# Kernel tuning notes

Hardware: AMD Instinct MI355X
Metric: run time of the kernel (lower is better)

## Reference

```python
import jax, jax.numpy as jnp
import numpy as np

B, N, DIN, DOUT, EIN, EOUT = 8, 256, 64, 64, 64, 64


def setup_inputs() -> dict:
    key = jax.random.key(0)
    ks = jax.random.split(key, 9)
    A = jax.random.randint(ks[0], (B, N, N), 0, 2).astype(jnp.float32)  # {0,1} connectivity
    emb_node = jax.random.normal(ks[1], (B, N, DIN), dtype=jnp.float32)
    emb_edge = jax.random.normal(ks[2], (B, N, N, EIN), dtype=jnp.float32)
    s_n = 1.0 / np.sqrt(DIN)
    s_e = 1.0 / np.sqrt(EIN)
    Wn = jax.random.uniform(ks[3], (DIN, DOUT), minval=-s_n, maxval=s_n)
    bn = jax.random.uniform(ks[4], (DOUT,), minval=-s_n, maxval=s_n)
    Wsn = jax.random.uniform(ks[5], (DIN, DOUT), minval=-s_n, maxval=s_n)
    bsn = jax.random.uniform(ks[6], (DOUT,), minval=-s_n, maxval=s_n)
    We = jax.random.uniform(ks[7], (EIN, EOUT), minval=-s_e, maxval=s_e)
    be = jax.random.uniform(ks[8], (EOUT,), minval=-s_e, maxval=s_e)
    return {"A": A, "emb_node": emb_node, "emb_edge": emb_edge,
            "Wn": Wn, "bn": bn, "Wsn": Wsn, "bsn": bsn, "We": We, "be": be}


def reference(A, emb_node, emb_edge, Wn, bn, Wsn, bsn, We, be):
    # mode=1 (default) of ChannelIndependentConv
    node_x = emb_node @ Wn + bn          # [B,N,DOUT]
    node_sx = emb_node @ Wsn + bsn       # [B,N,DOUT]
    edge_x = emb_edge @ We + be          # [B,N,N,EOUT]
    # mask edges by connectivity, then channel-independent aggregation:
    # out[b,i,c] = sum_j A[b,i,j] * edge_x[b,i,j,c] * node_x[b,j,c]
    Ae = A[..., None] * edge_x           # [B,N,N,EOUT]
    agg = jnp.einsum('bijc,bjc->bic', Ae, node_x)  # [B,N,DOUT]
    node_out = jax.nn.relu(agg) + jax.nn.relu(node_sx)
    edge_out = jax.nn.relu(edge_x)
    return node_out, edge_out
```

## Files before the change

kernel.cpp:

```cpp
#include <hip/hip_runtime.h>
#include <hip/hip_bf16.h>

#define BN   2048
#define NN   256
#define CH   64
#define RPC  32
#define NCHK 8
#define LDST 88

typedef __attribute__((ext_vector_type(8))) short short8;
typedef __attribute__((ext_vector_type(4))) short short4v;
typedef __attribute__((ext_vector_type(4))) float fv4;

static __device__ inline short f2bf(float f) {
  unsigned u = __float_as_uint(f);
  u += 0x7FFF + ((u >> 16) & 1);
  return (short)(u >> 16);
}
static __device__ inline short4v cvt4(fv4 v) {
  short4v r;
  r[0] = f2bf(v[0]); r[1] = f2bf(v[1]); r[2] = f2bf(v[2]); r[3] = f2bf(v[3]);
  return r;
}

__global__ __launch_bounds__(256) void node_kernel(
    const float* __restrict__ emb_node, const float* __restrict__ Wn,
    const float* __restrict__ bn, const float* __restrict__ Wsn,
    const float* __restrict__ bsn, float* __restrict__ node_x,
    float* __restrict__ rsx) {
  __shared__ float s_emb[4][CH];
  __shared__ float s_Wn[CH * CH];
  __shared__ float s_Ws[CH * CH];
  const int tid = threadIdx.x;
  const int r = tid >> 6;
  const int c = tid & 63;
  const int row = blockIdx.x * 4 + r;
#pragma unroll
  for (int i = 0; i < 4; ++i) {
    *(fv4*)&s_Wn[(i * 256 + tid) * 4] = *(const fv4*)&Wn[(i * 256 + tid) * 4];
    *(fv4*)&s_Ws[(i * 256 + tid) * 4] = *(const fv4*)&Wsn[(i * 256 + tid) * 4];
  }
  s_emb[r][c] = emb_node[row * CH + c];
  __syncthreads();
  float a1 = bn[c], a2 = bsn[c];
#pragma unroll
  for (int k = 0; k < CH; ++k) {
    const float e = s_emb[r][k];
    a1 = fmaf(e, s_Wn[k * CH + c], a1);
    a2 = fmaf(e, s_Ws[k * CH + c], a2);
  }
  node_x[row * CH + c] = a1;
  rsx[row * CH + c] = fmaxf(a2, 0.0f);
}

__global__ __launch_bounds__(256) void edge_mfma_kernel(
    const float* __restrict__ A, const float* __restrict__ emb_edge,
    const float* __restrict__ We, const float* __restrict__ be,
    const float* __restrict__ node_x, const float* __restrict__ rsx,
    float* __restrict__ node_out, float* __restrict__ edge_out) {
  const int bi   = blockIdx.x;
  const int b    = bi >> 8;
  const int tid  = threadIdx.x;
  const int lane = tid & 63;
  const int wave = tid >> 6;
  const int l15  = lane & 15;
  const int quad = lane >> 4;
  const int c    = wave * 16 + l15;

  __shared__ __align__(16) short sbuf[2][RPC * LDST];
  __shared__ float s_A[NN];

  short8 bfrag[2];
#pragma unroll
  for (int h = 0; h < 2; ++h)
#pragma unroll
    for (int j = 0; j < 8; ++j)
      bfrag[h][j] = f2bf(We[(h * 32 + quad * 8 + j) * CH + c]);
  const float bias = be[c];

  const float* __restrict__ ee = emb_edge + (size_t)bi * NN * CH;
  float*       __restrict__ eo = edge_out + (size_t)bi * NN * CH;
  const float* __restrict__ nx = node_x + (size_t)b * NN * CH;

  s_A[tid] = A[(size_t)bi * NN + tid];

  const int srow = tid >> 4;
  const int kcol = (tid & 15) * 4;

  fv4 st0 = *(const fv4*)(ee + tid * 4);
  fv4 st1 = *(const fv4*)(ee + 1024 + tid * 4);
  *(short4v*)&sbuf[0][srow * LDST + kcol] = cvt4(st0);
  *(short4v*)&sbuf[0][(16 + srow) * LDST + kcol] = cvt4(st1);

  float agg = 0.0f;

#pragma unroll 2
  for (int ch = 0; ch < NCHK; ++ch) {
    const int pb = ch & 1;
    if (ch + 1 < NCHK) {
      const float* cb = ee + (ch + 1) * (RPC * CH);
      st0 = *(const fv4*)(cb + tid * 4);
      st1 = *(const fv4*)(cb + 1024 + tid * 4);
    }
    __syncthreads();

#pragma unroll
    for (int half = 0; half < 2; ++half) {
      const int j0l = half * 16;
      const int j0  = ch * RPC + j0l;
      const fv4 av = *(const fv4*)&s_A[j0 + quad * 4];
      float nxv[4];
#pragma unroll
      for (int r = 0; r < 4; ++r)
        nxv[r] = nx[(j0 + quad * 4 + r) * CH + c];
      const short8 af0 =
          *(const short8*)&sbuf[pb][(j0l + l15) * LDST + quad * 8];
      const short8 af1 =
          *(const short8*)&sbuf[pb][(j0l + l15) * LDST + 32 + quad * 8];
      fv4 acc = {0.0f, 0.0f, 0.0f, 0.0f};
      acc = __builtin_amdgcn_mfma_f32_16x16x32_bf16(af0, bfrag[0], acc, 0, 0, 0);
      acc = __builtin_amdgcn_mfma_f32_16x16x32_bf16(af1, bfrag[1], acc, 0, 0, 0);
#pragma unroll
      for (int r = 0; r < 4; ++r) {
        const int row = j0 + quad * 4 + r;
        const float ex = acc[r] + bias;
        eo[row * CH + c] = fmaxf(ex, 0.0f);
        agg = fmaf(av[r] * ex, nxv[r], agg);
      }
    }

    if (ch + 1 < NCHK) {
      *(short4v*)&sbuf[pb ^ 1][srow * LDST + kcol] = cvt4(st0);
      *(short4v*)&sbuf[pb ^ 1][(16 + srow) * LDST + kcol] = cvt4(st1);
    }
  }

  agg += __shfl_xor(agg, 16, 64);
  agg += __shfl_xor(agg, 32, 64);
  if (quad == 0) {
    node_out[(size_t)bi * CH + c] =
        fmaxf(agg, 0.0f) + rsx[(size_t)bi * CH + c];
  }
}

extern "C" void kernel_launch(void* const* d_in, const int* in_sizes, int n_in,
                              void* d_out, int out_size, void* d_ws, size_t ws_size,
                              hipStream_t stream) {
  const float* A        = (const float*)d_in[0];
  const float* emb_node = (const float*)d_in[1];
  const float* emb_edge = (const float*)d_in[2];
  const float* Wn       = (const float*)d_in[3];
  const float* bn       = (const float*)d_in[4];
  const float* Wsn      = (const float*)d_in[5];
  const float* bsn      = (const float*)d_in[6];
  const float* We       = (const float*)d_in[7];
  const float* be       = (const float*)d_in[8];

  float* node_out = (float*)d_out;
  float* edge_out = (float*)d_out + (size_t)BN * CH;

  float* node_x = (float*)d_ws;
  float* rsx    = (float*)d_ws + (size_t)BN * CH;

  hipLaunchKernelGGL(node_kernel, dim3(BN / 4), dim3(256), 0, stream,
                     emb_node, Wn, bn, Wsn, bsn, node_x, rsx);
  hipLaunchKernelGGL(edge_mfma_kernel, dim3(BN), dim3(256), 0, stream,
                     A, emb_edge, We, be, node_x, rsx, node_out, edge_out);
}
```

Before: 258.0 us.

## Split edge rows across waves, load A-fragments directly, drop LDS staging

Restructures the edge kernel so each wave owns 64 rows and computes all 64 output channels. The wave loads its emb_edge fragments straight from global memory into registers and converts them to bf16 there, which removes the LDS double buffer and the per-chunk barriers. The bias is folded into the accumulator init, edge_out uses nontemporal stores, and a small LDS reduction combines the per-wave aggregates at the end. The cost is more registers for four sets of We fragments and scattered 32-byte global loads in place of coalesced staging loads.

Result: slower. 273.6 us (+6.1%).

```diff
diff --git a/kernel.cpp b/kernel.cpp
--- a/kernel.cpp
+++ b/kernel.cpp
@@ -1,15 +1,10 @@
 #include <hip/hip_runtime.h>
-#include <hip/hip_bf16.h>
 
 #define BN   2048
 #define NN   256
 #define CH   64
-#define RPC  32
-#define NCHK 8
-#define LDST 88
 
 typedef __attribute__((ext_vector_type(8))) short short8;
-typedef __attribute__((ext_vector_type(4))) short short4v;
 typedef __attribute__((ext_vector_type(4))) float fv4;
 
 static __device__ inline short f2bf(float f) {
@@ -17,9 +12,10 @@
   u += 0x7FFF + ((u >> 16) & 1);
   return (short)(u >> 16);
 }
-static __device__ inline short4v cvt4(fv4 v) {
-  short4v r;
-  r[0] = f2bf(v[0]); r[1] = f2bf(v[1]); r[2] = f2bf(v[2]); r[3] = f2bf(v[3]);
+static __device__ inline short8 cvt8(fv4 a, fv4 b) {
+  short8 r;
+  r[0] = f2bf(a[0]); r[1] = f2bf(a[1]); r[2] = f2bf(a[2]); r[3] = f2bf(a[3]);
+  r[4] = f2bf(b[0]); r[5] = f2bf(b[1]); r[6] = f2bf(b[2]); r[7] = f2bf(b[3]);
   return r;
 }
 
@@ -53,7 +49,7 @@
   rsx[row * CH + c] = fmaxf(a2, 0.0f);
 }
 
-__global__ __launch_bounds__(256) void edge_mfma_kernel(
+__global__ __launch_bounds__(256, 4) void edge_mfma_kernel(
     const float* __restrict__ A, const float* __restrict__ emb_edge,
     const float* __restrict__ We, const float* __restrict__ be,
     const float* __restrict__ node_x, const float* __restrict__ rsx,
@@ -65,81 +61,92 @@
   const int wave = tid >> 6;
   const int l15  = lane & 15;
   const int quad = lane >> 4;
-  const int c    = wave * 16 + l15;
 
-  __shared__ __align__(16) short sbuf[2][RPC * LDST];
-  __shared__ float s_A[NN];
+  __shared__ float s_red[4][CH];
 
-  short8 bfrag[2];
+  short8 bf[4][2];
+  float  beL[4];
 #pragma unroll
-  for (int h = 0; h < 2; ++h)
+  for (int tc = 0; tc < 4; ++tc) {
+    const int c = tc * 16 + l15;
+    beL[tc] = be[c];
 #pragma unroll
-    for (int j = 0; j < 8; ++j)
-      bfrag[h][j] = f2bf(We[(h * 32 + quad * 8 + j) * CH + c]);
-  const float bias = be[c];
+    for (int h = 0; h < 2; ++h)
+#pragma unroll
+      for (int j = 0; j < 8; ++j)
+        bf[tc][h][j] = f2bf(We[(h * 32 + quad * 8 + j) * CH + c]);
+  }
 
   const float* __restrict__ ee = emb_edge + (size_t)bi * NN * CH;
   float*       __restrict__ eo = edge_out + (size_t)bi * NN * CH;
   const float* __restrict__ nx = node_x + (size_t)b * NN * CH;
+  const float* __restrict__ Ar = A + (size_t)bi * NN;
 
-  s_A[tid] = A[(size_t)bi * NN + tid];
+  const int wbase = wave * 64;
+  float agg[4] = {0.f, 0.f, 0.f, 0.f};
 
-  const int srow = tid >> 4;
-  const int kcol = (tid & 15) * 4;
+  fv4 x0, x1, x2, x3, y0, y1, y2, y3;
 
-  fv4 st0 = *(const fv4*)(ee + tid * 4);
-  fv4 st1 = *(const fv4*)(ee + 1024 + tid * 4);
-  *(short4v*)&sbuf[0][srow * LDST + kcol] = cvt4(st0);
-  *(short4v*)&sbuf[0][(16 + srow) * LDST + kcol] = cvt4(st1);
+#define LOADT(T, A0, A1, A2, A3)                                             \
+  {                                                                          \
+    const float* rp = ee + (wbase + (T) * 16 + l15) * CH + quad * 8;         \
+    A0 = *(const fv4*)rp;        A1 = *(const fv4*)(rp + 4);                 \
+    A2 = *(const fv4*)(rp + 32); A3 = *(const fv4*)(rp + 36);                \
+  }
 
-  float agg = 0.0f;
+#define COMPT(T, A0, A1, A2, A3)                                             \
+  {                                                                          \
+    const int j0 = wbase + (T) * 16;                                         \
+    const int rb = j0 + quad * 4;                                            \
+    const fv4 av = *(const fv4*)(Ar + rb);                                   \
+    const float* nxp = nx + rb * CH + l15;                                   \
+    float nxv[4][4];                                                         \
+    _Pragma("unroll") for (int tc = 0; tc < 4; ++tc)                         \
+      _Pragma("unroll") for (int r = 0; r < 4; ++r)                          \
+        nxv[tc][r] = nxp[r * CH + tc * 16];              \
+    const short8 af0 = cvt8(A0, A1);                                         \
+    const short8 af1 = cvt8(A2, A3);                                         \
+    _Pragma("unroll") for (int tc = 0; tc < 4; ++tc) {                       \
+      fv4 acc = {beL[tc], beL[tc], beL[tc], beL[tc]};      \
+      acc = __builtin_amdgcn_mfma_f32_16x16x32_bf16(af0, bf[tc][0], acc, 0, 0, 0); \
+      acc = __builtin_amdgcn_mfma_f32_16x16x32_bf16(af1, bf[tc][1], acc, 0, 0, 0); \
+      _Pragma("unroll") for (int r = 0; r < 4; ++r) {                        \
+        const int row = rb + r;                                              \
+        const float ex = acc[r];                        \
+        __builtin_nontemporal_store(fmaxf(ex, 0.f),                          \
+                                    eo + row * CH + tc * 16 + l15);          \
+        agg[tc] = fmaf(av[r] * ex, nxv[tc][r], agg[tc]);                     \
+      }                                                                      \
+    }                                                                        \
+  }
 
-#pragma unroll 2
-  for (int ch = 0; ch < NCHK; ++ch) {
-    const int pb = ch & 1;
-    if (ch + 1 < NCHK) {
-      const float* cb = ee + (ch + 1) * (RPC * CH);
-      st0 = *(const fv4*)(cb + tid * 4);
-      st1 = *(const fv4*)(cb + 1024 + tid * 4);
-    }
-    __syncthreads();
+  LOADT(0, x0, x1, x2, x3);
+  LOADT(1, y0, y1, y2, y3);
+  COMPT(0, x0, x1, x2, x3);
+  LOADT(2, x0, x1, x2, x3);
+  COMPT(1, y0, y1, y2, y3);
+  LOADT(3, y0, y1, y2, y3);
+  COMPT(2, x0, x1, x2, x3);
+  COMPT(3, y0, y1, y2, y3);
+
+#undef LOADT
+#undef COMPT
 
 #pragma unroll
-    for (int half = 0; half < 2; ++half) {
-      const int j0l = half * 16;
-      const int j0  = ch * RPC + j0l;
-      const fv4 av = *(const fv4*)&s_A[j0 + quad * 4];
-      float nxv[4];
+  for (int tc = 0; tc < 4; ++tc) {
+    agg[tc] += __shfl_xor(agg[tc], 16, 64);
+    agg[tc] += __shfl_xor(agg[tc], 32, 64);
+  }
+  if (quad == 0) {
 #pragma unroll
-      for (int r = 0; r < 4; ++r)
-        nxv[r] = nx[(j0 + quad * 4 + r) * CH + c];
-      const short8 af0 =
-          *(const short8*)&sbuf[pb][(j0l + l15) * LDST + quad * 8];
-      const short8 af1 =
-          *(const short8*)&sbuf[pb][(j0l + l15) * LDST + 32 + quad * 8];
-      fv4 acc = {0.0f, 0.0f, 0.0f, 0.0f};
-      acc = __builtin_amdgcn_mfma_f32_16x16x32_bf16(af0, bfrag[0], acc, 0, 0, 0);
-      acc = __builtin_amdgcn_mfma_f32_16x16x32_bf16(af1, bfrag[1], acc, 0, 0, 0);
-#pragma unroll
-      for (int r = 0; r < 4; ++r) {
-        const int row = j0 + quad * 4 + r;
-        const float ex = acc[r] + bias;
-        eo[row * CH + c] = fmaxf(ex, 0.0f);
-        agg = fmaf(av[r] * ex, nxv[r], agg);
-      }
-    }
-
-    if (ch + 1 < NCHK) {
-      *(short4v*)&sbuf[pb ^ 1][srow * LDST + kcol] = cvt4(st0);
-      *(short4v*)&sbuf[pb ^ 1][(16 + srow) * LDST + kcol] = cvt4(st1);
-    }
+    for (int tc = 0; tc < 4; ++tc) s_red[wave][tc * 16 + l15] = agg[tc];
   }
-
-  agg += __shfl_xor(agg, 16, 64);
-  agg += __shfl_xor(agg, 32, 64);
-  if (quad == 0) {
-    node_out[(size_t)bi * CH + c] =
-        fmaxf(agg, 0.0f) + rsx[(size_t)bi * CH + c];
+  __syncthreads();
+  if (tid < CH) {
+    const float s =
+        s_red[0][tid] + s_red[1][tid] + s_red[2][tid] + s_red[3][tid];
+    node_out[(size_t)bi * CH + tid] =
+        fmaxf(s, 0.f) + rsx[(size_t)bi * CH + tid];
   }
 }
 
```

## Deepen edge-kernel prefetch to three chunks and prefetch node_x one chunk ahead

Applied to the files above, without the earlier changes.

Turns the single-stage register prefetch of edge rows into a three-deep ring of register buffers, so global loads are issued three chunks ahead. node_x values are also prefetched one chunk ahead, the chunk loop is fully unrolled, and the bias is folded into the MFMA accumulator init. __syncthreads is replaced with an explicit LDS waitcnt plus s_barrier so outstanding global loads are not drained at each barrier. The goal is to hide HBM latency in this memory-bound kernel, at the cost of more registers under a launch bound of 4 blocks, which could spill or lower occupancy.

After: 260.1 us. Within noise of the previous version (+0.8%).

```diff
diff --git a/kernel.cpp b/kernel.cpp
--- a/kernel.cpp
+++ b/kernel.cpp
@@ -1,5 +1,4 @@
 #include <hip/hip_runtime.h>
-#include <hip/hip_bf16.h>
 
 #define BN   2048
 #define NN   256
@@ -53,7 +52,7 @@
   rsx[row * CH + c] = fmaxf(a2, 0.0f);
 }
 
-__global__ __launch_bounds__(256) void edge_mfma_kernel(
+__global__ __launch_bounds__(256, 4) void edge_mfma_kernel(
     const float* __restrict__ A, const float* __restrict__ emb_edge,
     const float* __restrict__ We, const float* __restrict__ be,
     const float* __restrict__ node_x, const float* __restrict__ rsx,
@@ -70,68 +69,98 @@
   __shared__ __align__(16) short sbuf[2][RPC * LDST];
   __shared__ float s_A[NN];
 
+  const float* __restrict__ ee = emb_edge + (size_t)bi * NN * CH;
+  float*       __restrict__ eo = edge_out + (size_t)bi * NN * CH;
+  const float* __restrict__ nx = node_x + (size_t)b * NN * CH;
+
+  const float aval = A[(size_t)bi * NN + tid];
+  float wraw[16];
+#pragma unroll
+  for (int h = 0; h < 2; ++h)
+#pragma unroll
+    for (int j = 0; j < 8; ++j)
+      wraw[h * 8 + j] = We[(h * 32 + quad * 8 + j) * CH + c];
+  const float bias = be[c];
+
+  const int srow = tid >> 4;
+  const int kcol = (tid & 15) * 4;
+
+  fv4 st[3][2];
+  st[0][0] = *(const fv4*)(ee + tid * 4);
+  st[0][1] = *(const fv4*)(ee + 1024 + tid * 4);
+
+  float nxv[2][8];
+#pragma unroll
+  for (int h = 0; h < 2; ++h)
+#pragma unroll
+    for (int r = 0; r < 4; ++r)
+      nxv[0][h * 4 + r] = nx[(h * 16 + quad * 4 + r) * CH + c];
+
+  st[1][0] = *(const fv4*)(ee + 2048 + tid * 4);
+  st[1][1] = *(const fv4*)(ee + 3072 + tid * 4);
+  st[2][0] = *(const fv4*)(ee + 4096 + tid * 4);
+  st[2][1] = *(const fv4*)(ee + 5120 + tid * 4);
+
+  s_A[tid] = aval;
+
   short8 bfrag[2];
 #pragma unroll
   for (int h = 0; h < 2; ++h)
 #pragma unroll
     for (int j = 0; j < 8; ++j)
-      bfrag[h][j] = f2bf(We[(h * 32 + quad * 8 + j) * CH + c]);
-  const float bias = be[c];
+      bfrag[h][j] = f2bf(wraw[h * 8 + j]);
 
-  const float* __restrict__ ee = emb_edge + (size_t)bi * NN * CH;
-  float*       __restrict__ eo = edge_out + (size_t)bi * NN * CH;
-  const float* __restrict__ nx = node_x + (size_t)b * NN * CH;
-
-  s_A[tid] = A[(size_t)bi * NN + tid];
-
-  const int srow = tid >> 4;
-  const int kcol = (tid & 15) * 4;
-
-  fv4 st0 = *(const fv4*)(ee + tid * 4);
-  fv4 st1 = *(const fv4*)(ee + 1024 + tid * 4);
-  *(short4v*)&sbuf[0][srow * LDST + kcol] = cvt4(st0);
-  *(short4v*)&sbuf[0][(16 + srow) * LDST + kcol] = cvt4(st1);
+  *(short4v*)&sbuf[0][srow * LDST + kcol] = cvt4(st[0][0]);
+  *(short4v*)&sbuf[0][(16 + srow) * LDST + kcol] = cvt4(st[0][1]);
 
   float agg = 0.0f;
 
-#pragma unroll 2
+#pragma unroll
   for (int ch = 0; ch < NCHK; ++ch) {
     const int pb = ch & 1;
+
     if (ch + 1 < NCHK) {
-      const float* cb = ee + (ch + 1) * (RPC * CH);
-      st0 = *(const fv4*)(cb + tid * 4);
-      st1 = *(const fv4*)(cb + 1024 + tid * 4);
+#pragma unroll
+      for (int h = 0; h < 2; ++h)
+#pragma unroll
+        for (int r = 0; r < 4; ++r)
+          nxv[(ch + 1) & 1][h * 4 + r] =
+              nx[((ch + 1) * RPC + h * 16 + quad * 4 + r) * CH + c];
     }
-    __syncthreads();
+    if (ch + 3 < NCHK) {
+      const float* cb = ee + (ch + 3) * (RPC * CH);
+      st[ch % 3][0] = *(const fv4*)(cb + tid * 4);
+      st[ch % 3][1] = *(const fv4*)(cb + 1024 + tid * 4);
+    }
+
+    asm volatile("s_waitcnt lgkmcnt(0)" ::: "memory");
+    __builtin_amdgcn_s_barrier();
 
 #pragma unroll
-    for (int half = 0; half < 2; ++half) {
-      const int j0l = half * 16;
+    for (int h = 0; h < 2; ++h) {
+      const int j0l = h * 16;
       const int j0  = ch * RPC + j0l;
       const fv4 av = *(const fv4*)&s_A[j0 + quad * 4];
-      float nxv[4];
-#pragma unroll
-      for (int r = 0; r < 4; ++r)
-        nxv[r] = nx[(j0 + quad * 4 + r) * CH + c];
       const short8 af0 =
           *(const short8*)&sbuf[pb][(j0l + l15) * LDST + quad * 8];
       const short8 af1 =
           *(const short8*)&sbuf[pb][(j0l + l15) * LDST + 32 + quad * 8];
-      fv4 acc = {0.0f, 0.0f, 0.0f, 0.0f};
+      fv4 acc = {bias, bias, bias, bias};
       acc = __builtin_amdgcn_mfma_f32_16x16x32_bf16(af0, bfrag[0], acc, 0, 0, 0);
       acc = __builtin_amdgcn_mfma_f32_16x16x32_bf16(af1, bfrag[1], acc, 0, 0, 0);
 #pragma unroll
       for (int r = 0; r < 4; ++r) {
         const int row = j0 + quad * 4 + r;
-        const float ex = acc[r] + bias;
+        const float ex = acc[r];
         eo[row * CH + c] = fmaxf(ex, 0.0f);
-        agg = fmaf(av[r] * ex, nxv[r], agg);
+        agg = fmaf(av[r] * ex, nxv[ch & 1][h * 4 + r], agg);
       }
     }
 
     if (ch + 1 < NCHK) {
-      *(short4v*)&sbuf[pb ^ 1][srow * LDST + kcol] = cvt4(st0);
-      *(short4v*)&sbuf[pb ^ 1][(16 + srow) * LDST + kcol] = cvt4(st1);
+      *(short4v*)&sbuf[pb ^ 1][srow * LDST + kcol] = cvt4(st[(ch + 1) % 3][0]);
+      *(short4v*)&sbuf[pb ^ 1][(16 + srow) * LDST + kcol] =
+          cvt4(st[(ch + 1) % 3][1]);
     }
   }
 
```

## Stage edge and node tiles via direct global-to-LDS loads with triple buffering

Applied to the files above, without the earlier changes.

Replaces the register-staged, bf16-converted double buffer with global_load_lds transfers of raw fp32 edge and node_x tiles into a three-deep, XOR-swizzled shared-memory ring. Waits use explicit vmcnt counts and barriers. Conversion to bf16 moves to the MFMA operand read and uses packed cvt instructions, and the bias is folded into the accumulator init. The aim is deeper prefetch and removing the register round trip and uncoalesced node_x reads, at the cost of larger LDS use, which may limit occupancy, and fragile hand-tuned wait counts.

Measured after the change: 258.2 us. Within noise of the previous version (+0.1%).

```diff
diff --git a/kernel.cpp b/kernel.cpp
--- a/kernel.cpp
+++ b/kernel.cpp
@@ -1,15 +1,11 @@
 #include <hip/hip_runtime.h>
-#include <hip/hip_bf16.h>
 
 #define BN   2048
 #define NN   256
 #define CH   64
-#define RPC  32
 #define NCHK 8
-#define LDST 88
 
 typedef __attribute__((ext_vector_type(8))) short short8;
-typedef __attribute__((ext_vector_type(4))) short short4v;
 typedef __attribute__((ext_vector_type(4))) float fv4;
 
 static __device__ inline short f2bf(float f) {
@@ -17,11 +13,22 @@
   u += 0x7FFF + ((u >> 16) & 1);
   return (short)(u >> 16);
 }
-static __device__ inline short4v cvt4(fv4 v) {
-  short4v r;
-  r[0] = f2bf(v[0]); r[1] = f2bf(v[1]); r[2] = f2bf(v[2]); r[3] = f2bf(v[3]);
-  return r;
-}
+
+static __device__ inline short8 cvt_frag(fv4 a, fv4 b) {
+  union { short8 s; unsigned u[4]; } r;
+  asm("v_cvt_pk_bf16_f32 %0, %1, %2" : "=v"(r.u[0]) : "v"(a[0]), "v"(a[1]));
+  asm("v_cvt_pk_bf16_f32 %0, %1, %2" : "=v"(r.u[1]) : "v"(a[2]), "v"(a[3]));
+  asm("v_cvt_pk_bf16_f32 %0, %1, %2" : "=v"(r.u[2]) : "v"(b[0]), "v"(b[1]));
+  asm("v_cvt_pk_bf16_f32 %0, %1, %2" : "=v"(r.u[3]) : "v"(b[2]), "v"(b[3]));
+  return r.s;
+}
+
+#define GLOAD16(gp, lp)                                                        \
+  __builtin_amdgcn_global_load_lds(                                            \
+      (const __attribute__((address_space(1))) unsigned*)(gp),                 \
+      (__attribute__((address_space(3))) unsigned*)(lp), 16, 0, 0)
+
+#define WAITV(N) asm volatile("s_waitcnt vmcnt(" #N ")" ::: "memory")
 
 __global__ __launch_bounds__(256) void node_kernel(
     const float* __restrict__ emb_node, const float* __restrict__ Wn,
@@ -53,7 +60,7 @@
   rsx[row * CH + c] = fmaxf(a2, 0.0f);
 }
 
-__global__ __launch_bounds__(256) void edge_mfma_kernel(
+__global__ __launch_bounds__(256, 4) void edge_mfma_kernel(
     const float* __restrict__ A, const float* __restrict__ emb_edge,
     const float* __restrict__ We, const float* __restrict__ be,
     const float* __restrict__ node_x, const float* __restrict__ rsx,
@@ -67,8 +74,16 @@
   const int quad = lane >> 4;
   const int c    = wave * 16 + l15;
 
-  __shared__ __align__(16) short sbuf[2][RPC * LDST];
-  __shared__ float s_A[NN];
+  __shared__ __align__(16) float s_e[3][2048];
+  __shared__ __align__(16) float s_n[3][2048];
+  __shared__ __align__(16) float s_Af[NN];
+
+  const float* __restrict__ ee = emb_edge + (size_t)bi * NN * CH;
+  float*       __restrict__ eo = edge_out + (size_t)bi * NN * CH;
+  const float* __restrict__ nx = node_x + (size_t)b * NN * CH;
+
+  const float aval = A[(size_t)bi * NN + tid];
+  s_Af[tid] = aval;
 
   short8 bfrag[2];
 #pragma unroll
@@ -78,62 +93,88 @@
       bfrag[h][j] = f2bf(We[(h * 32 + quad * 8 + j) * CH + c]);
   const float bias = be[c];
 
-  const float* __restrict__ ee = emb_edge + (size_t)bi * NN * CH;
-  float*       __restrict__ eo = edge_out + (size_t)bi * NN * CH;
-  const float* __restrict__ nx = node_x + (size_t)b * NN * CH;
-
-  s_A[tid] = A[(size_t)bi * NN + tid];
-
-  const int srow = tid >> 4;
-  const int kcol = (tid & 15) * 4;
-
-  fv4 st0 = *(const fv4*)(ee + tid * 4);
-  fv4 st1 = *(const fv4*)(ee + 1024 + tid * 4);
-  *(short4v*)&sbuf[0][srow * LDST + kcol] = cvt4(st0);
-  *(short4v*)&sbuf[0][(16 + srow) * LDST + kcol] = cvt4(st1);
+  const int rowA = wave * 8 + (lane >> 4);
+  const int rowB = rowA + 4;
+  const int ibq  = (lane & 15) * 16;
+  const int offA = rowA * 256 + (ibq ^ ((rowA & 15) << 4));
+  const int offB = rowB * 256 + (ibq ^ ((rowB & 15) << 4));
+  const int swz = l15 << 4;
+  const int o0 = (quad * 32) ^ swz;
+  const int o1 = (quad * 32 + 16) ^ swz;
+  const int o2 = (128 + quad * 32) ^ swz;
+  const int o3 = (144 + quad * 32) ^ swz;
+  int nxo[4];
+#pragma unroll
+  for (int r = 0; r < 4; ++r)
+    nxo[r] = (quad * 4 + r) * 256 + ((c * 4) ^ ((quad * 4 + r) << 4));
+
+#define STAGE(T, D)                                                            \
+  {                                                                            \
+    const char* eb_ = (const char*)ee + (T) * 8192;                            \
+    const char* nb_ = (const char*)nx + (T) * 8192;                            \
+    GLOAD16(eb_ + offA, (char*)&s_e[(D)][0] + wave * 2048);                    \
+    GLOAD16(eb_ + offB, (char*)&s_e[(D)][0] + wave * 2048 + 1024);             \
+    GLOAD16(nb_ + offA, (char*)&s_n[(D)][0] + wave * 2048);                    \
+    GLOAD16(nb_ + offB, (char*)&s_n[(D)][0] + wave * 2048 + 1024);             \
+  }
+
+  STAGE(0, 0)
+  STAGE(1, 1)
 
   float agg = 0.0f;
 
-#pragma unroll 2
-  for (int ch = 0; ch < NCHK; ++ch) {
-    const int pb = ch & 1;
-    if (ch + 1 < NCHK) {
-      const float* cb = ee + (ch + 1) * (RPC * CH);
-      st0 = *(const fv4*)(cb + tid * 4);
-      st1 = *(const fv4*)(cb + 1024 + tid * 4);
-    }
-    __syncthreads();
-
-#pragma unroll
-    for (int half = 0; half < 2; ++half) {
-      const int j0l = half * 16;
-      const int j0  = ch * RPC + j0l;
-      const fv4 av = *(const fv4*)&s_A[j0 + quad * 4];
-      float nxv[4];
-#pragma unroll
-      for (int r = 0; r < 4; ++r)
-        nxv[r] = nx[(j0 + quad * 4 + r) * CH + c];
-      const short8 af0 =
-          *(const short8*)&sbuf[pb][(j0l + l15) * LDST + quad * 8];
-      const short8 af1 =
-          *(const short8*)&sbuf[pb][(j0l + l15) * LDST + 32 + quad * 8];
-      fv4 acc = {0.0f, 0.0f, 0.0f, 0.0f};
-      acc = __builtin_amdgcn_mfma_f32_16x16x32_bf16(af0, bfrag[0], acc, 0, 0, 0);
-      acc = __builtin_amdgcn_mfma_f32_16x16x32_bf16(af1, bfrag[1], acc, 0, 0, 0);
-#pragma unroll
-      for (int r = 0; r < 4; ++r) {
-        const int row = j0 + quad * 4 + r;
-        const float ex = acc[r] + bias;
-        eo[row * CH + c] = fmaxf(ex, 0.0f);
-        agg = fmaf(av[r] * ex, nxv[r], agg);
-      }
-    }
-
-    if (ch + 1 < NCHK) {
-      *(short4v*)&sbuf[pb ^ 1][srow * LDST + kcol] = cvt4(st0);
-      *(short4v*)&sbuf[pb ^ 1][(16 + srow) * LDST + kcol] = cvt4(st1);
-    }
-  }
+#define COMPUTE(CHK, D)                                                        \
+  {                                                                            \
+    _Pragma("unroll") for (int h = 0; h < 2; ++h) {                            \
+      const char* eb_ = (const char*)&s_e[(D)][0] + (h * 16 + l15) * 256;      \
+      const fv4 a0 = *(const fv4*)(eb_ + o0);                                  \
+      const fv4 a1 = *(const fv4*)(eb_ + o1);                                  \
+      const fv4 a2 = *(const fv4*)(eb_ + o2);                                  \
+      const fv4 a3 = *(const fv4*)(eb_ + o3);                                  \
+      const short8 af0 = cvt_frag(a0, a1);                                     \
+      const short8 af1 = cvt_frag(a2, a3);                                     \
+      fv4 acc = {bias, bias, bias, bias};                                      \
+      acc = __builtin_amdgcn_mfma_f32_16x16x32_bf16(af0, bfrag[0], acc, 0,0,0);\
+      acc = __builtin_amdgcn_mfma_f32_16x16x32_bf16(af1, bfrag[1], acc, 0,0,0);\
+      const int j0 = (CHK) * 32 + h * 16;                                      \
+      const fv4 av = *(const fv4*)&s_Af[j0 + quad * 4];                        \
+      const char* nb_ = (const char*)&s_n[(D)][0] + h * 4096;                  \
+      _Pragma("unroll") for (int r = 0; r < 4; ++r) {                          \
+        const float nxv = *(const float*)(nb_ + nxo[r]);                       \
+        const int row = j0 + quad * 4 + r;                                     \
+        const float ex = acc[r];                          \
+        eo[row * CH + c] = fmaxf(ex, 0.0f);                                    \
+        agg = fmaf(av[r] * ex, nxv, agg);                                      \
+      }                                                                        \
+    }                                                                          \
+  }
+
+#define ITER(CHK, NW, PF)                                                      \
+  {                                                                            \
+    WAITV(NW);                                                                 \
+    __builtin_amdgcn_s_barrier();                                              \
+    if (PF) STAGE((CHK) + 2, ((CHK) + 2) % 3)                                  \
+    asm volatile("" ::: "memory");                 \
+    COMPUTE(CHK, (CHK) % 3)                                                    \
+  }
+
+  asm volatile("s_waitcnt vmcnt(4) lgkmcnt(0)" ::: "memory");
+  __builtin_amdgcn_s_barrier();
+  STAGE(2, 2)
+  asm volatile("" ::: "memory");
+  COMPUTE(0, 0)
+
+  ITER(1, 12, 1)
+  ITER(2, 20, 1)
+  ITER(3, 20, 1)
+  ITER(4, 20, 1)
+  ITER(5, 20, 1)
+  ITER(6, 20, 0)
+  ITER(7, 16, 0)
+
+#undef ITER
+#undef COMPUTE
+#undef STAGE
 
   agg += __shfl_xor(agg, 16, 64);
   agg += __shfl_xor(agg, 32, 64);
```
